# Optimization experiments

Measured on AMD Instinct MI355X. Metric: run time of the kernel, lower is better.

The kernel has to match this reference:

```python
import jax, jax.numpy as jnp
import numpy as np

B, C, H, W = 8, 128, 64, 64
KC = 32  # key_channels

def setup_inputs() -> dict:
    key = jax.random.key(0)
    ks = jax.random.split(key, 6)
    s = lambda fan_in: 1.0 / np.sqrt(fan_in)
    x  = jax.random.normal(ks[0], (B, C, H, W), dtype=jnp.float32)
    Wq = jax.random.uniform(ks[1], (KC, C), jnp.float32, -s(C), s(C))  # 1x1 conv kernels
    Wk = jax.random.uniform(ks[2], (KC, C), jnp.float32, -s(C), s(C))
    Wv = jax.random.uniform(ks[3], (C, C), jnp.float32, -s(C), s(C))
    Wo = jax.random.uniform(ks[4], (C, C), jnp.float32, -s(C), s(C))
    gamma = jnp.zeros((1,), jnp.float32) + 0.1  # nonzero so attention path matters
    return {"x": x, "Wq": Wq, "Wk": Wk, "Wv": Wv, "Wo": Wo, "gamma": gamma}

def reference(x, Wq, Wk, Wv, Wo, gamma):
    b, c, h, w = x.shape
    xf = x.reshape(b, c, h * w)                      # [B,C,N]
    Q = jnp.einsum('qc,bcn->bnq', Wq, xf)            # [B,N,KC]
    K = jnp.einsum('kc,bcn->bkn', Wk, xf)            # [B,KC,N]
    V = jnp.einsum('vc,bcn->bnv', Wv, xf)            # [B,N,C]
    scores = jnp.einsum('bnq,bqm->bnm', Q, K) / jnp.sqrt(jnp.asarray(Wq.shape[0], x.dtype))
    attn = jax.nn.softmax(scores, axis=-1)           # [B,N,N]
    out = jnp.einsum('bnm,bmv->bvn', attn, V)        # [B,C,N]
    out = jnp.einsum('oc,bcn->bon', Wo, out).reshape(b, c, h, w)
    return x + gamma * out
```

## Files before the change

kernel.cpp:

```cpp
#include <hip/hip_runtime.h>
#include <hip/hip_bf16.h>

#define BB 8
#define CC 128
#define NN 4096
#define KCQ 32

typedef unsigned short u16;
typedef unsigned int u32;
typedef unsigned char u8;
typedef __bf16 bf16x8 __attribute__((ext_vector_type(8)));
typedef float f32x4 __attribute__((ext_vector_type(4)));
typedef long i64;

typedef const __attribute__((address_space(1))) void gas_t;
typedef __attribute__((address_space(3))) void las_t;

__device__ __forceinline__ u16 f2bf(float f){
  u32 u = __builtin_bit_cast(u32, f);
  u32 r = u + 0x7FFFu + ((u >> 16) & 1u);
  return (u16)(r >> 16);
}
__device__ __forceinline__ u32 cvtpk(float lo, float hi){
  u32 r; asm("v_cvt_pk_bf16_f32 %0, %1, %2" : "=v"(r) : "v"(lo), "v"(hi)); return r;
}
__device__ __forceinline__ u32 pk_fp8x4(float a, float b, float c, float d){
  int v = 0;
  v = __builtin_amdgcn_cvt_pk_fp8_f32(a, b, v, false);
  v = __builtin_amdgcn_cvt_pk_fp8_f32(c, d, v, true);
  return (u32)v;
}
__device__ __forceinline__ void gload16(const void* g, void* l){
  __builtin_amdgcn_global_load_lds((gas_t*)g, (las_t*)l, 16, 0, 0);
}

__global__ __launch_bounds__(256) void k_prep_w(const float* Wq, const float* Wk,
                                                const float* Wv, const float* Wo,
                                                u16* wsq, u16* wsk, u16* wsv, u16* wso){
  int i = blockIdx.x * 256 + threadIdx.x;
  const float SC = 0.2550350f;
  if (i < 4096)       wsq[i]        = f2bf(Wq[i] * SC);
  else if (i < 8192)  wsk[i-4096]   = f2bf(Wk[i-4096]);
  else if (i < 24576) wsv[i-8192]   = f2bf(Wv[i-8192]);
  else if (i < 40960) wso[i-24576]  = f2bf(Wo[i-24576]);
}

__global__ __launch_bounds__(512) void k_projx(const float* x, const u16* wq, const u16* wk,
                                               const u16* wv, u16* Qm, u16* Km, u8* Vt8){
  __shared__ __align__(16) u16 xL[64*132];
  int b = blockIdx.x >> 6, nb = (blockIdx.x & 63) * 64;
  int t = threadIdx.x;
  int n = t & 63, cg = t >> 6;
  #pragma unroll
  for (int it = 0; it < 16; ++it){
    int c = it*8 + cg;
    xL[n*132 + c] = f2bf(x[((size_t)b*CC + c)*NN + nb + n]);
  }
  __syncthreads();
  int w = t >> 6, l = t & 63, a = l & 15, g = l >> 4;
  int ns = w >> 1, half = w & 1;
  int n0 = nb + ns*16;
  bf16x8 xa[4];
  #pragma unroll
  for (int kc = 0; kc < 4; ++kc)
    xa[kc] = *(const bf16x8*)(xL + (ns*16 + a)*132 + kc*32 + g*8);
  __syncthreads();

  u32* vbuf = (u32*)xL;
  auto Vjob = [&](int vt){
    f32x4 acc = {0.f,0.f,0.f,0.f};
    #pragma unroll
    for (int kc = 0; kc < 4; ++kc){
      bf16x8 wa = ((const bf16x8*)(wv + (size_t)(vt*16 + a) * CC))[kc*4 + g];
      acc = __builtin_amdgcn_mfma_f32_16x16x32_bf16(xa[kc], wa, acc, 0,0,0);
    }
    int row = vt*16 + a;
    vbuf[row*16 + ((ns ^ ((a>>1)&3)) << 2) + g] = pk_fp8x4(acc[0], acc[1], acc[2], acc[3]);
  };

  if (half == 0){
    #pragma unroll
    for (int qt = 0; qt < 2; ++qt){
      f32x4 accq = {0.f,0.f,0.f,0.f}, acck = {0.f,0.f,0.f,0.f};
      #pragma unroll
      for (int kc = 0; kc < 4; ++kc){
        bf16x8 wbq = ((const bf16x8*)(wq + (size_t)(qt*16 + a) * CC))[kc*4 + g];
        bf16x8 wbk = ((const bf16x8*)(wk + (size_t)(qt*16 + a) * CC))[kc*4 + g];
        accq = __builtin_amdgcn_mfma_f32_16x16x32_bf16(xa[kc], wbq, accq, 0,0,0);
        acck = __builtin_amdgcn_mfma_f32_16x16x32_bf16(xa[kc], wbk, acck, 0,0,0);
      }
      #pragma unroll
      for (int r = 0; r < 4; ++r){
        Qm[((size_t)b*NN + n0 + 4*g + r) * KCQ + qt*16 + a] = f2bf(accq[r]);
        Km[((size_t)b*NN + n0 + 4*g + r) * KCQ + qt*16 + a] = f2bf(acck[r]);
      }
    }
    Vjob(0); Vjob(1);
  } else {
    #pragma unroll
    for (int vt = 2; vt < 8; ++vt) Vjob(vt);
  }
  __syncthreads();
  {
    int row = t >> 2, ck = t & 3, key = (row >> 1) & 3;
    uint4 d = ((const uint4*)vbuf)[row*4 + (ck ^ key)];
    *(uint4*)(Vt8 + ((size_t)b*CC + row)*NN + nb + ck*16) = d;
  }
}

__global__ __launch_bounds__(512, 4) void k_attn(const u16* Qm, const u16* Km,
                                                 const u8* Vt8, const u16* wso,
                                                 const float* x, const float* gamma,
                                                 float* out){
  __shared__ __align__(16) char smem[65536];
  int bid = blockIdx.x;
  int b = bid & 7, qb = bid >> 3;
  int t0 = threadIdx.x;
  int l = t0 & 63, a = l & 15, g = l >> 4;
  int w = t0 >> 6, h = w >> 2, wq = w & 3;
  int q0 = qb * 64;
  int kb0 = h * 2048;

  const u8* Vb = Vt8 + (size_t)b * CC * NN;

  bf16x8 qf[4];
  #pragma unroll
  for (int qs = 0; qs < 4; ++qs)
    qf[qs] = ((const bf16x8*)(Qm + ((size_t)b*NN + q0 + qs*16 + a) * KCQ))[g];
  const u16* kPtr = Km + ((size_t)b*NN + kb0 + wq*16 + a) * KCQ + g*8;

  f32x4 o[8];
  #pragma unroll
  for (int i = 0; i < 8; ++i) o[i] = (f32x4){0.f,0.f,0.f,0.f};
  float ls[4] = {0.f, 0.f, 0.f, 0.f};

  int schk = (l&3) ^ ((l>>3)&3);
  const u8* vSrc = Vb + (size_t)(wq*32 + (l>>2))*NN + kb0 + (schk << 4);
  int vOff = h*8192 + wq*2048 + l*16;
  auto stageV = [&](int t1, int sl){
    const u8* vs = vSrc + t1*64;
    char* vd = smem + sl*16384 + vOff;
    gload16(vs, vd);
    gload16(vs + (size_t)16*NN, vd + 1024);
  };

  const int cswz = (a >> 1) & 3;
  auto PV = [&](int ps, int vsl){
    const char* Vs = smem + vsl*16384 + h*8192;
    const char* Pr = smem + 49152 + ps*8192 + h*4096;
    __builtin_amdgcn_s_setprio(1);
    #pragma unroll
    for (int kk = 0; kk < 2; ++kk){
      int kx = (((kk*2 + (g>>1)) ^ cswz) << 4) + (g&1)*8;
      i64 vf0 = *(const i64*)(Vs + (wq*32 + a)*64 + kx);
      i64 vf1 = *(const i64*)(Vs + (wq*32 + 16 + a)*64 + kx);
      i64 pf[4];
      #pragma unroll
      for (int qs = 0; qs < 4; ++qs)
        pf[qs] = *(const i64*)(Pr + (qs*16 + a)*64 + kx);
      #pragma unroll
      for (int qs = 0; qs < 4; ++qs){
        o[qs*2  ] = __builtin_amdgcn_mfma_f32_16x16x32_fp8_fp8(vf0, pf[qs], o[qs*2  ], 0,0,0);
        o[qs*2+1] = __builtin_amdgcn_mfma_f32_16x16x32_fp8_fp8(vf1, pf[qs], o[qs*2+1], 0,0,0);
      }
    }
    __builtin_amdgcn_s_setprio(0);
  };

  stageV(0, 0);
  bf16x8 kfC = *(const bf16x8*)(kPtr);

  int vS = 1, vR = 2;
  for (int t = 0; t < 32; ++t){
    bf16x8 kfN;
    if (t < 31){
      kfN = *(const bf16x8*)(kPtr + (size_t)(t+1)*2048);
      stageV(t+1, vS);
    }
    f32x4 sv[4];
    #pragma unroll
    for (int qs = 0; qs < 4; ++qs){
      f32x4 z = {0.f,0.f,0.f,0.f};
      sv[qs] = __builtin_amdgcn_mfma_f32_16x16x32_bf16(kfC, qf[qs], z, 0,0,0);
    }
    if (t > 0) PV((t&1)^1, vR);
    char* Pw = smem + 49152 + (t&1)*8192 + h*4096;
    #pragma unroll
    for (int qs = 0; qs < 4; ++qs){
      float p0 = __builtin_amdgcn_exp2f(sv[qs][0]);
      float p1 = __builtin_amdgcn_exp2f(sv[qs][1]);
      float p2 = __builtin_amdgcn_exp2f(sv[qs][2]);
      float p3 = __builtin_amdgcn_exp2f(sv[qs][3]);
      ls[qs] += (p0 + p1) + (p2 + p3);
      *(u32*)(Pw + (qs*16 + a)*64 + ((wq ^ cswz) << 4) + 4*g) = pk_fp8x4(p0, p1, p2, p3);
    }
    if (t < 31) { asm volatile("s_waitcnt vmcnt(3) lgkmcnt(0)" ::: "memory"); }
    else        { asm volatile("s_waitcnt vmcnt(0) lgkmcnt(0)" ::: "memory"); }
    __builtin_amdgcn_s_barrier();
    kfC = kfN;
    vR = (vR == 2) ? 0 : vR + 1;
    vS = (vS == 2) ? 0 : vS + 1;
  }
  PV(1, vR);

  #pragma unroll
  for (int qs = 0; qs < 4; ++qs){
    ls[qs] += __shfl_xor(ls[qs], 16);
    ls[qs] += __shfl_xor(ls[qs], 32);
  }
  float* Ml = (float*)(smem + 36864);
  if (l < 16){
    #pragma unroll
    for (int qs = 0; qs < 4; ++qs) Ml[w*64 + qs*16 + l] = ls[qs];
  }
  float* Cx = (float*)smem;
  __syncthreads();
  if (h == 1){
    #pragma unroll
    for (int i = 0; i < 8; ++i){
      int qs = i >> 1, st = i & 1;
      *(f32x4*)(Cx + (qs*16 + a)*132 + wq*32 + st*16 + 4*g) = o[i];
    }
  }
  __syncthreads();
  u16* Ol = (u16*)(smem + 49152);
  if (h == 0){
    #pragma unroll
    for (int qs = 0; qs < 4; ++qs){
      float lsum = 0.f;
      #pragma unroll
      for (int ww = 0; ww < 8; ++ww) lsum += Ml[ww*64 + qs*16 + a];
      float inv = 1.f / lsum;
      #pragma unroll
      for (int st = 0; st < 2; ++st){
        f32x4 oc = o[qs*2 + st];
        const float* cx = Cx + (qs*16 + a)*132 + wq*32 + st*16 + 4*g;
        uint2 pk;
        pk.x = cvtpk((oc[0] + cx[0]) * inv, (oc[1] + cx[1]) * inv);
        pk.y = cvtpk((oc[2] + cx[2]) * inv, (oc[3] + cx[3]) * inv);
        int chunk = (wq*4 + st*2 + (g>>1)) ^ (a & 7);
        *(uint2*)((char*)Ol + (qs*16 + a)*256 + chunk*16 + (g&1)*8) = pk;
      }
    }
  }
  __syncthreads();
  float gm = gamma[0];
  f32x4 acc2[4];
  #pragma unroll
  for (int qs = 0; qs < 4; ++qs) acc2[qs] = (f32x4){0.f,0.f,0.f,0.f};
  #pragma unroll
  for (int kc = 0; kc < 4; ++kc){
    bf16x8 wof = *(const bf16x8*)(wso + (size_t)(w*16 + a)*CC + kc*32 + g*8);
    #pragma unroll
    for (int qs = 0; qs < 4; ++qs){
      int chunk = (kc*4 + g) ^ (a & 7);
      bf16x8 of = *(const bf16x8*)((const char*)Ol + (qs*16 + a)*256 + chunk*16);
      acc2[qs] = __builtin_amdgcn_mfma_f32_16x16x32_bf16(wof, of, acc2[qs], 0,0,0);
    }
  }
  #pragma unroll
  for (int qs = 0; qs < 4; ++qs){
    #pragma unroll
    for (int r = 0; r < 4; ++r){
      size_t idx = ((size_t)b*CC + w*16 + 4*g + r)*NN + q0 + qs*16 + a;
      out[idx] = x[idx] + gm * acc2[qs][r];
    }
  }
}

extern "C" void kernel_launch(void* const* d_in, const int* in_sizes, int n_in,
                              void* d_out, int out_size, void* d_ws, size_t ws_size,
                              hipStream_t stream) {
  const float* x     = (const float*)d_in[0];
  const float* Wq    = (const float*)d_in[1];
  const float* Wk    = (const float*)d_in[2];
  const float* Wv    = (const float*)d_in[3];
  const float* Wo    = (const float*)d_in[4];
  const float* gamma = (const float*)d_in[5];
  float* out = (float*)d_out;

  u16* wsq = (u16*)d_ws;
  u16* wsk = wsq + 4096;
  u16* wsv = wsk + 4096;
  u16* wso = wsv + 16384;
  u16* Qm  = wso + 16384;
  u16* Km  = Qm + (size_t)BB*NN*KCQ;
  u8*  Vt8 = (u8*)(Km + (size_t)BB*NN*KCQ);

  hipLaunchKernelGGL(k_prep_w, dim3(160), dim3(256), 0, stream, Wq, Wk, Wv, Wo, wsq, wsk, wsv, wso);
  hipLaunchKernelGGL(k_projx,  dim3(512), dim3(512), 0, stream, x, wsq, wsk, wsv, Qm, Km, Vt8);
  hipLaunchKernelGGL(k_attn,   dim3(512), dim3(512), 0, stream, Qm, Km, Vt8, wso, x, gamma, out);
}
```

Measured before the change: 73.03 us.

## Restructure attention kernel to 32-query blocks with direct V register loads

Each attention block now handles 32 queries with 4 waves instead of 64 queries with 8 waves. The two-half key split, with its cross-half reduction of partial outputs through shared memory, is gone. V fp8 fragments are loaded straight from global memory into registers each iteration instead of being staged into LDS with a triple-buffered async copy, so LDS use drops to about 8.5 KB and the grid doubles to 1024 blocks. The aim is higher occupancy and less LDS traffic, at the cost of reading the full V of the batch twice as often from cache and exposing global load latency inside the loop.

```diff
diff --git a/kernel.cpp b/kernel.cpp
--- a/kernel.cpp
+++ b/kernel.cpp
@@ -13,9 +13,6 @@
 typedef float f32x4 __attribute__((ext_vector_type(4)));
 typedef long i64;
 
-typedef const __attribute__((address_space(1))) void gas_t;
-typedef __attribute__((address_space(3))) void las_t;
-
 __device__ __forceinline__ u16 f2bf(float f){
   u32 u = __builtin_bit_cast(u32, f);
   u32 r = u + 0x7FFFu + ((u >> 16) & 1u);
@@ -29,9 +26,6 @@
   v = __builtin_amdgcn_cvt_pk_fp8_f32(a, b, v, false);
   v = __builtin_amdgcn_cvt_pk_fp8_f32(c, d, v, true);
   return (u32)v;
-}
-__device__ __forceinline__ void gload16(const void* g, void* l){
-  __builtin_amdgcn_global_load_lds((gas_t*)g, (las_t*)l, 16, 0, 0);
 }
 
 __global__ __launch_bounds__(256) void k_prep_w(const float* Wq, const float* Wk,
@@ -108,164 +102,142 @@
   }
 }
 
-__global__ __launch_bounds__(512, 4) void k_attn(const u16* Qm, const u16* Km,
+__global__ __launch_bounds__(256, 4) void k_attn(const u16* Qm, const u16* Km,
                                                  const u8* Vt8, const u16* wso,
                                                  const float* x, const float* gamma,
                                                  float* out){
-  __shared__ __align__(16) char smem[65536];
+  __shared__ __align__(16) char smem[8704];
   int bid = blockIdx.x;
   int b = bid & 7, qb = bid >> 3;
   int t0 = threadIdx.x;
   int l = t0 & 63, a = l & 15, g = l >> 4;
-  int w = t0 >> 6, h = w >> 2, wq = w & 3;
-  int q0 = qb * 64;
-  int kb0 = h * 2048;
-
-  const u8* Vb = Vt8 + (size_t)b * CC * NN;
-
-  bf16x8 qf[4];
-  #pragma unroll
-  for (int qs = 0; qs < 4; ++qs)
+  int w = t0 >> 6;
+  int q0 = qb * 32;
+
+  bf16x8 qf[2];
+  #pragma unroll
+  for (int qs = 0; qs < 2; ++qs)
     qf[qs] = ((const bf16x8*)(Qm + ((size_t)b*NN + q0 + qs*16 + a) * KCQ))[g];
-  const u16* kPtr = Km + ((size_t)b*NN + kb0 + wq*16 + a) * KCQ + g*8;
-
-  f32x4 o[8];
-  #pragma unroll
-  for (int i = 0; i < 8; ++i) o[i] = (f32x4){0.f,0.f,0.f,0.f};
-  float ls[4] = {0.f, 0.f, 0.f, 0.f};
-
-  int schk = (l&3) ^ ((l>>3)&3);
-  const u8* vSrc = Vb + (size_t)(wq*32 + (l>>2))*NN + kb0 + (schk << 4);
-  int vOff = h*8192 + wq*2048 + l*16;
-  auto stageV = [&](int t1, int sl){
-    const u8* vs = vSrc + t1*64;
-    char* vd = smem + sl*16384 + vOff;
-    gload16(vs, vd);
-    gload16(vs + (size_t)16*NN, vd + 1024);
-  };
-
-  const int cswz = (a >> 1) & 3;
-  auto PV = [&](int ps, int vsl){
-    const char* Vs = smem + vsl*16384 + h*8192;
-    const char* Pr = smem + 49152 + ps*8192 + h*4096;
+
+  const u16* kPtr = Km + ((size_t)b*NN + w*32 + a) * KCQ + g*8;
+  const u8*  vP0  = Vt8 + ((size_t)b*CC + w*32 + a) * NN + g*8;
+  const u8*  vP1  = vP0 + (size_t)16 * NN;
+
+  f32x4 o[4];
+  #pragma unroll
+  for (int i = 0; i < 4; ++i) o[i] = (f32x4){0.f,0.f,0.f,0.f};
+  float ls[2] = {0.f, 0.f};
+
+  const int sx = (a & 7) << 4;
+  bf16x8 kfC[2];
+  kfC[0] = *(const bf16x8*)(kPtr);
+  kfC[1] = *(const bf16x8*)(kPtr + 512);
+
+  for (int t = 0; t < 32; ++t){
+    i64 vf[8];
+    #pragma unroll
+    for (int kk = 0; kk < 4; ++kk){
+      vf[kk]     = *(const i64*)(vP0 + t*128 + kk*32);
+      vf[4 + kk] = *(const i64*)(vP1 + t*128 + kk*32);
+    }
+    bf16x8 kfN[2];
+    kfN[0] = *(const bf16x8*)(kPtr + (size_t)(t+1)*4096);
+    kfN[1] = *(const bf16x8*)(kPtr + (size_t)(t+1)*4096 + 512);
+
+    f32x4 sv[4];
+    #pragma unroll
+    for (int su = 0; su < 2; ++su)
+      #pragma unroll
+      for (int qs = 0; qs < 2; ++qs){
+        f32x4 z = {0.f,0.f,0.f,0.f};
+        sv[su*2+qs] = __builtin_amdgcn_mfma_f32_16x16x32_bf16(kfC[su], qf[qs], z, 0,0,0);
+      }
+    char* Pw = smem + (t&1)*4096;
+    #pragma unroll
+    for (int su = 0; su < 2; ++su)
+      #pragma unroll
+      for (int qs = 0; qs < 2; ++qs){
+        f32x4 s = sv[su*2+qs];
+        float p0 = __builtin_amdgcn_exp2f(s[0]);
+        float p1 = __builtin_amdgcn_exp2f(s[1]);
+        float p2 = __builtin_amdgcn_exp2f(s[2]);
+        float p3 = __builtin_amdgcn_exp2f(s[3]);
+        ls[qs] += (p0 + p1) + (p2 + p3);
+        *(u32*)(Pw + (qs*16 + a)*128 + (((w*2 + su) << 4) ^ sx) + 4*g) =
+            pk_fp8x4(p0, p1, p2, p3);
+      }
+    asm volatile("s_waitcnt lgkmcnt(0)" ::: "memory");
+    __builtin_amdgcn_s_barrier();
+
+    const char* Pr = Pw;
     __builtin_amdgcn_s_setprio(1);
     #pragma unroll
-    for (int kk = 0; kk < 2; ++kk){
-      int kx = (((kk*2 + (g>>1)) ^ cswz) << 4) + (g&1)*8;
-      i64 vf0 = *(const i64*)(Vs + (wq*32 + a)*64 + kx);
-      i64 vf1 = *(const i64*)(Vs + (wq*32 + 16 + a)*64 + kx);
-      i64 pf[4];
-      #pragma unroll
-      for (int qs = 0; qs < 4; ++qs)
-        pf[qs] = *(const i64*)(Pr + (qs*16 + a)*64 + kx);
-      #pragma unroll
-      for (int qs = 0; qs < 4; ++qs){
-        o[qs*2  ] = __builtin_amdgcn_mfma_f32_16x16x32_fp8_fp8(vf0, pf[qs], o[qs*2  ], 0,0,0);
-        o[qs*2+1] = __builtin_amdgcn_mfma_f32_16x16x32_fp8_fp8(vf1, pf[qs], o[qs*2+1], 0,0,0);
-      }
+    for (int kk = 0; kk < 4; ++kk){
+      int kx = (((kk*2 + (g>>1)) << 4) ^ sx) + (g&1)*8;
+      i64 pf0 = *(const i64*)(Pr + a*128 + kx);
+      i64 pf1 = *(const i64*)(Pr + (16 + a)*128 + kx);
+      o[0] = __builtin_amdgcn_mfma_f32_16x16x32_fp8_fp8(vf[kk],   pf0, o[0], 0,0,0);
+      o[1] = __builtin_amdgcn_mfma_f32_16x16x32_fp8_fp8(vf[kk],   pf1, o[1], 0,0,0);
+      o[2] = __builtin_amdgcn_mfma_f32_16x16x32_fp8_fp8(vf[4+kk], pf0, o[2], 0,0,0);
+      o[3] = __builtin_amdgcn_mfma_f32_16x16x32_fp8_fp8(vf[4+kk], pf1, o[3], 0,0,0);
     }
     __builtin_amdgcn_s_setprio(0);
-  };
-
-  stageV(0, 0);
-  bf16x8 kfC = *(const bf16x8*)(kPtr);
-
-  int vS = 1, vR = 2;
-  for (int t = 0; t < 32; ++t){
-    bf16x8 kfN;
-    if (t < 31){
-      kfN = *(const bf16x8*)(kPtr + (size_t)(t+1)*2048);
-      stageV(t+1, vS);
-    }
-    f32x4 sv[4];
-    #pragma unroll
-    for (int qs = 0; qs < 4; ++qs){
-      f32x4 z = {0.f,0.f,0.f,0.f};
-      sv[qs] = __builtin_amdgcn_mfma_f32_16x16x32_bf16(kfC, qf[qs], z, 0,0,0);
-    }
-    if (t > 0) PV((t&1)^1, vR);
-    char* Pw = smem + 49152 + (t&1)*8192 + h*4096;
-    #pragma unroll
-    for (int qs = 0; qs < 4; ++qs){
-      float p0 = __builtin_amdgcn_exp2f(sv[qs][0]);
-      float p1 = __builtin_amdgcn_exp2f(sv[qs][1]);
-      float p2 = __builtin_amdgcn_exp2f(sv[qs][2]);
-      float p3 = __builtin_amdgcn_exp2f(sv[qs][3]);
-      ls[qs] += (p0 + p1) + (p2 + p3);
-      *(u32*)(Pw + (qs*16 + a)*64 + ((wq ^ cswz) << 4) + 4*g) = pk_fp8x4(p0, p1, p2, p3);
-    }
-    if (t < 31) { asm volatile("s_waitcnt vmcnt(3) lgkmcnt(0)" ::: "memory"); }
-    else        { asm volatile("s_waitcnt vmcnt(0) lgkmcnt(0)" ::: "memory"); }
-    __builtin_amdgcn_s_barrier();
-    kfC = kfN;
-    vR = (vR == 2) ? 0 : vR + 1;
-    vS = (vS == 2) ? 0 : vS + 1;
-  }
-  PV(1, vR);
-
-  #pragma unroll
-  for (int qs = 0; qs < 4; ++qs){
+    kfC[0] = kfN[0]; kfC[1] = kfN[1];
+  }
+
+  #pragma unroll
+  for (int qs = 0; qs < 2; ++qs){
     ls[qs] += __shfl_xor(ls[qs], 16);
     ls[qs] += __shfl_xor(ls[qs], 32);
   }
-  float* Ml = (float*)(smem + 36864);
+  float* Ml = (float*)(smem + 8192);
+  __syncthreads();
   if (l < 16){
-    #pragma unroll
-    for (int qs = 0; qs < 4; ++qs) Ml[w*64 + qs*16 + l] = ls[qs];
-  }
-  float* Cx = (float*)smem;
-  __syncthreads();
-  if (h == 1){
-    #pragma unroll
-    for (int i = 0; i < 8; ++i){
-      int qs = i >> 1, st = i & 1;
-      *(f32x4*)(Cx + (qs*16 + a)*132 + wq*32 + st*16 + 4*g) = o[i];
-    }
-  }
-  __syncthreads();
-  u16* Ol = (u16*)(smem + 49152);
-  if (h == 0){
-    #pragma unroll
-    for (int qs = 0; qs < 4; ++qs){
-      float lsum = 0.f;
-      #pragma unroll
-      for (int ww = 0; ww < 8; ++ww) lsum += Ml[ww*64 + qs*16 + a];
-      float inv = 1.f / lsum;
-      #pragma unroll
-      for (int st = 0; st < 2; ++st){
-        f32x4 oc = o[qs*2 + st];
-        const float* cx = Cx + (qs*16 + a)*132 + wq*32 + st*16 + 4*g;
-        uint2 pk;
-        pk.x = cvtpk((oc[0] + cx[0]) * inv, (oc[1] + cx[1]) * inv);
-        pk.y = cvtpk((oc[2] + cx[2]) * inv, (oc[3] + cx[3]) * inv);
-        int chunk = (wq*4 + st*2 + (g>>1)) ^ (a & 7);
-        *(uint2*)((char*)Ol + (qs*16 + a)*256 + chunk*16 + (g&1)*8) = pk;
-      }
+    Ml[w*32 + l]      = ls[0];
+    Ml[w*32 + 16 + l] = ls[1];
+  }
+  __syncthreads();
+  u16* Ol = (u16*)smem;
+  #pragma unroll
+  for (int qs = 0; qs < 2; ++qs){
+    float lsum = Ml[qs*16 + a] + Ml[32 + qs*16 + a] + Ml[64 + qs*16 + a] + Ml[96 + qs*16 + a];
+    float inv = 1.f / lsum;
+    #pragma unroll
+    for (int st = 0; st < 2; ++st){
+      f32x4 oc = o[st*2 + qs];
+      uint2 pk;
+      pk.x = cvtpk(oc[0]*inv, oc[1]*inv);
+      pk.y = cvtpk(oc[2]*inv, oc[3]*inv);
+      int chunk = (w*4 + st*2 + (g>>1)) ^ (a & 7);
+      *(uint2*)((char*)Ol + (qs*16 + a)*256 + chunk*16 + (g&1)*8) = pk;
     }
   }
   __syncthreads();
   float gm = gamma[0];
   f32x4 acc2[4];
   #pragma unroll
-  for (int qs = 0; qs < 4; ++qs) acc2[qs] = (f32x4){0.f,0.f,0.f,0.f};
+  for (int i = 0; i < 4; ++i) acc2[i] = (f32x4){0.f,0.f,0.f,0.f};
   #pragma unroll
   for (int kc = 0; kc < 4; ++kc){
-    bf16x8 wof = *(const bf16x8*)(wso + (size_t)(w*16 + a)*CC + kc*32 + g*8);
-    #pragma unroll
-    for (int qs = 0; qs < 4; ++qs){
+    bf16x8 wof0 = *(const bf16x8*)(wso + (size_t)(w*32 + a)*CC + kc*32 + g*8);
+    bf16x8 wof1 = *(const bf16x8*)(wso + (size_t)(w*32 + 16 + a)*CC + kc*32 + g*8);
+    #pragma unroll
+    for (int qs = 0; qs < 2; ++qs){
       int chunk = (kc*4 + g) ^ (a & 7);
       bf16x8 of = *(const bf16x8*)((const char*)Ol + (qs*16 + a)*256 + chunk*16);
-      acc2[qs] = __builtin_amdgcn_mfma_f32_16x16x32_bf16(wof, of, acc2[qs], 0,0,0);
-    }
-  }
-  #pragma unroll
-  for (int qs = 0; qs < 4; ++qs){
-    #pragma unroll
-    for (int r = 0; r < 4; ++r){
-      size_t idx = ((size_t)b*CC + w*16 + 4*g + r)*NN + q0 + qs*16 + a;
-      out[idx] = x[idx] + gm * acc2[qs][r];
-    }
-  }
+      acc2[qs]     = __builtin_amdgcn_mfma_f32_16x16x32_bf16(wof0, of, acc2[qs],     0,0,0);
+      acc2[2 + qs] = __builtin_amdgcn_mfma_f32_16x16x32_bf16(wof1, of, acc2[2 + qs], 0,0,0);
+    }
+  }
+  #pragma unroll
+  for (int st = 0; st < 2; ++st)
+    #pragma unroll
+    for (int qs = 0; qs < 2; ++qs)
+      #pragma unroll
+      for (int r = 0; r < 4; ++r){
+        size_t idx = ((size_t)b*CC + w*32 + st*16 + 4*g + r)*NN + q0 + qs*16 + a;
+        out[idx] = x[idx] + gm * acc2[st*2 + qs][r];
+      }
 }
 
 extern "C" void kernel_launch(void* const* d_in, const int* in_sizes, int n_in,
@@ -287,7 +259,7 @@
   u16* Km  = Qm + (size_t)BB*NN*KCQ;
   u8*  Vt8 = (u8*)(Km + (size_t)BB*NN*KCQ);
 
-  hipLaunchKernelGGL(k_prep_w, dim3(160), dim3(256), 0, stream, Wq, Wk, Wv, Wo, wsq, wsk, wsv, wso);
-  hipLaunchKernelGGL(k_projx,  dim3(512), dim3(512), 0, stream, x, wsq, wsk, wsv, Qm, Km, Vt8);
-  hipLaunchKernelGGL(k_attn,   dim3(512), dim3(512), 0, stream, Qm, Km, Vt8, wso, x, gamma, out);
-}
+  hipLaunchKernelGGL(k_prep_w, dim3(160),  dim3(256), 0, stream, Wq, Wk, Wv, Wo, wsq, wsk, wsv, wso);
+  hipLaunchKernelGGL(k_projx,  dim3(512),  dim3(512), 0, stream, x, wsq, wsk, wsv, Qm, Km, Vt8);
+  hipLaunchKernelGGL(k_attn,   dim3(1024), dim3(256), 0, stream, Qm, Km, Vt8, wso, x, gamma, out);
+}
```

Result: slower. 161.5 us (+121.1%).

## Halve attention query tile to 32 and simplify V staging to double buffer

Applied to the files above, without the earlier changes.

The attention kernel now handles 32 queries per block instead of 64, doubling the grid to 1024 blocks and cutting LDS to 40KB with launch bounds raised to 8 waves per EU for more blocks per CU. The V pipeline moves from a triple-buffered prefetch, where PV lagged one step behind, to a double buffer: the next V tile is issued after the barrier and PV is consumed in the same iteration. This trades more K/V reloads per query (less reuse) for higher occupancy and a simpler schedule. It also risks exposing load latency, since the PV of each step now waits on the barrier.

```diff
diff --git a/kernel.cpp b/kernel.cpp
--- a/kernel.cpp
+++ b/kernel.cpp
@@ -108,85 +108,56 @@
   }
 }
 
-__global__ __launch_bounds__(512, 4) void k_attn(const u16* Qm, const u16* Km,
+__global__ __launch_bounds__(512, 8) void k_attn(const u16* Qm, const u16* Km,
                                                  const u8* Vt8, const u16* wso,
                                                  const float* x, const float* gamma,
                                                  float* out){
-  __shared__ __align__(16) char smem[65536];
+  __shared__ __align__(16) char smem[40960];
   int bid = blockIdx.x;
   int b = bid & 7, qb = bid >> 3;
   int t0 = threadIdx.x;
   int l = t0 & 63, a = l & 15, g = l >> 4;
   int w = t0 >> 6, h = w >> 2, wq = w & 3;
-  int q0 = qb * 64;
-  int kb0 = h * 2048;
-
-  const u8* Vb = Vt8 + (size_t)b * CC * NN;
-
-  bf16x8 qf[4];
-  #pragma unroll
-  for (int qs = 0; qs < 4; ++qs)
+  int q0 = qb * 32;
+
+  bf16x8 qf[2];
+  #pragma unroll
+  for (int qs = 0; qs < 2; ++qs)
     qf[qs] = ((const bf16x8*)(Qm + ((size_t)b*NN + q0 + qs*16 + a) * KCQ))[g];
-  const u16* kPtr = Km + ((size_t)b*NN + kb0 + wq*16 + a) * KCQ + g*8;
-
-  f32x4 o[8];
-  #pragma unroll
-  for (int i = 0; i < 8; ++i) o[i] = (f32x4){0.f,0.f,0.f,0.f};
-  float ls[4] = {0.f, 0.f, 0.f, 0.f};
+
+  const u16* kRun = Km + ((size_t)b*NN + h*2048 + wq*16 + a) * KCQ + g*8;
+
+  f32x4 o[4];
+  #pragma unroll
+  for (int i = 0; i < 4; ++i) o[i] = (f32x4){0.f,0.f,0.f,0.f};
+  float ls[2] = {0.f, 0.f};
 
   int schk = (l&3) ^ ((l>>3)&3);
-  const u8* vSrc = Vb + (size_t)(wq*32 + (l>>2))*NN + kb0 + (schk << 4);
-  int vOff = h*8192 + wq*2048 + l*16;
-  auto stageV = [&](int t1, int sl){
-    const u8* vs = vSrc + t1*64;
-    char* vd = smem + sl*16384 + vOff;
-    gload16(vs, vd);
-    gload16(vs + (size_t)16*NN, vd + 1024);
-  };
+  const u8* vRun = Vt8 + (size_t)b*CC*NN + (size_t)(wq*32 + (l>>2))*NN + h*2048 + schk*16;
+  const int vOff = h*8192 + wq*2048 + l*16;
+
+  {
+    char* vd = smem + vOff;
+    gload16(vRun, vd);
+    gload16(vRun + (size_t)16*NN, vd + 1024);
+    vRun += 64;
+  }
+  bf16x8 kfC = *(const bf16x8*)kRun; kRun += 2048;
 
   const int cswz = (a >> 1) & 3;
-  auto PV = [&](int ps, int vsl){
-    const char* Vs = smem + vsl*16384 + h*8192;
-    const char* Pr = smem + 49152 + ps*8192 + h*4096;
-    __builtin_amdgcn_s_setprio(1);
-    #pragma unroll
-    for (int kk = 0; kk < 2; ++kk){
-      int kx = (((kk*2 + (g>>1)) ^ cswz) << 4) + (g&1)*8;
-      i64 vf0 = *(const i64*)(Vs + (wq*32 + a)*64 + kx);
-      i64 vf1 = *(const i64*)(Vs + (wq*32 + 16 + a)*64 + kx);
-      i64 pf[4];
-      #pragma unroll
-      for (int qs = 0; qs < 4; ++qs)
-        pf[qs] = *(const i64*)(Pr + (qs*16 + a)*64 + kx);
-      #pragma unroll
-      for (int qs = 0; qs < 4; ++qs){
-        o[qs*2  ] = __builtin_amdgcn_mfma_f32_16x16x32_fp8_fp8(vf0, pf[qs], o[qs*2  ], 0,0,0);
-        o[qs*2+1] = __builtin_amdgcn_mfma_f32_16x16x32_fp8_fp8(vf1, pf[qs], o[qs*2+1], 0,0,0);
-      }
-    }
-    __builtin_amdgcn_s_setprio(0);
-  };
-
-  stageV(0, 0);
-  bf16x8 kfC = *(const bf16x8*)(kPtr);
-
-  int vS = 1, vR = 2;
+
   for (int t = 0; t < 32; ++t){
-    bf16x8 kfN;
-    if (t < 31){
-      kfN = *(const bf16x8*)(kPtr + (size_t)(t+1)*2048);
-      stageV(t+1, vS);
-    }
-    f32x4 sv[4];
-    #pragma unroll
-    for (int qs = 0; qs < 4; ++qs){
+    bf16x8 kfN = *(const bf16x8*)kRun; kRun += 2048;
+
+    f32x4 sv[2];
+    #pragma unroll
+    for (int qs = 0; qs < 2; ++qs){
       f32x4 z = {0.f,0.f,0.f,0.f};
       sv[qs] = __builtin_amdgcn_mfma_f32_16x16x32_bf16(kfC, qf[qs], z, 0,0,0);
     }
-    if (t > 0) PV((t&1)^1, vR);
-    char* Pw = smem + 49152 + (t&1)*8192 + h*4096;
-    #pragma unroll
-    for (int qs = 0; qs < 4; ++qs){
+    char* Pw = smem + 32768 + (t&1)*4096 + h*2048;
+    #pragma unroll
+    for (int qs = 0; qs < 2; ++qs){
       float p0 = __builtin_amdgcn_exp2f(sv[qs][0]);
       float p1 = __builtin_amdgcn_exp2f(sv[qs][1]);
       float p2 = __builtin_amdgcn_exp2f(sv[qs][2]);
@@ -194,46 +165,66 @@
       ls[qs] += (p0 + p1) + (p2 + p3);
       *(u32*)(Pw + (qs*16 + a)*64 + ((wq ^ cswz) << 4) + 4*g) = pk_fp8x4(p0, p1, p2, p3);
     }
-    if (t < 31) { asm volatile("s_waitcnt vmcnt(3) lgkmcnt(0)" ::: "memory"); }
+    if (t < 31) { asm volatile("s_waitcnt vmcnt(1) lgkmcnt(0)" ::: "memory"); }
     else        { asm volatile("s_waitcnt vmcnt(0) lgkmcnt(0)" ::: "memory"); }
     __builtin_amdgcn_s_barrier();
+
+    if (t < 31){
+      char* vd = smem + (((t+1)&1) << 14) + vOff;
+      gload16(vRun, vd);
+      gload16(vRun + (size_t)16*NN, vd + 1024);
+      vRun += 64;
+    }
+    const char* Vs = smem + ((t&1) << 14) + h*8192;
+    const char* Pr = smem + 32768 + (t&1)*4096 + h*2048;
+    __builtin_amdgcn_s_setprio(1);
+    #pragma unroll
+    for (int kk = 0; kk < 2; ++kk){
+      int kx = (((kk*2 + (g>>1)) ^ cswz) << 4) + (g&1)*8;
+      i64 pf0 = *(const i64*)(Pr + a*64 + kx);
+      i64 pf1 = *(const i64*)(Pr + (16 + a)*64 + kx);
+      i64 vf0 = *(const i64*)(Vs + (wq*32 + a)*64 + kx);
+      i64 vf1 = *(const i64*)(Vs + (wq*32 + 16 + a)*64 + kx);
+      o[0] = __builtin_amdgcn_mfma_f32_16x16x32_fp8_fp8(vf0, pf0, o[0], 0,0,0);
+      o[1] = __builtin_amdgcn_mfma_f32_16x16x32_fp8_fp8(vf0, pf1, o[1], 0,0,0);
+      o[2] = __builtin_amdgcn_mfma_f32_16x16x32_fp8_fp8(vf1, pf0, o[2], 0,0,0);
+      o[3] = __builtin_amdgcn_mfma_f32_16x16x32_fp8_fp8(vf1, pf1, o[3], 0,0,0);
+    }
+    __builtin_amdgcn_s_setprio(0);
     kfC = kfN;
-    vR = (vR == 2) ? 0 : vR + 1;
-    vS = (vS == 2) ? 0 : vS + 1;
-  }
-  PV(1, vR);
-
-  #pragma unroll
-  for (int qs = 0; qs < 4; ++qs){
+  }
+
+  #pragma unroll
+  for (int qs = 0; qs < 2; ++qs){
     ls[qs] += __shfl_xor(ls[qs], 16);
     ls[qs] += __shfl_xor(ls[qs], 32);
   }
-  float* Ml = (float*)(smem + 36864);
+  __syncthreads();
+  float* Ml = (float*)(smem + 32768);
   if (l < 16){
-    #pragma unroll
-    for (int qs = 0; qs < 4; ++qs) Ml[w*64 + qs*16 + l] = ls[qs];
+    Ml[w*32 + l]      = ls[0];
+    Ml[w*32 + 16 + l] = ls[1];
   }
   float* Cx = (float*)smem;
-  __syncthreads();
   if (h == 1){
     #pragma unroll
-    for (int i = 0; i < 8; ++i){
-      int qs = i >> 1, st = i & 1;
-      *(f32x4*)(Cx + (qs*16 + a)*132 + wq*32 + st*16 + 4*g) = o[i];
-    }
-  }
-  __syncthreads();
-  u16* Ol = (u16*)(smem + 49152);
+    for (int st = 0; st < 2; ++st)
+      #pragma unroll
+      for (int qs = 0; qs < 2; ++qs)
+        *(f32x4*)(Cx + (qs*16 + a)*132 + wq*32 + st*16 + 4*g) = o[st*2 + qs];
+  }
+  __syncthreads();
+  u16* Ol = (u16*)(smem + 17408);
   if (h == 0){
     #pragma unroll
-    for (int qs = 0; qs < 4; ++qs){
+    for (int qs = 0; qs < 2; ++qs){
       float lsum = 0.f;
       #pragma unroll
-      for (int ww = 0; ww < 8; ++ww) lsum += Ml[ww*64 + qs*16 + a];
+      for (int ww = 0; ww < 8; ++ww) lsum += Ml[ww*32 + qs*16 + a];
       float inv = 1.f / lsum;
       #pragma unroll
       for (int st = 0; st < 2; ++st){
-        f32x4 oc = o[qs*2 + st];
+        f32x4 oc = o[st*2 + qs];
         const float* cx = Cx + (qs*16 + a)*132 + wq*32 + st*16 + 4*g;
         uint2 pk;
         pk.x = cvtpk((oc[0] + cx[0]) * inv, (oc[1] + cx[1]) * inv);
@@ -245,27 +236,26 @@
   }
   __syncthreads();
   float gm = gamma[0];
-  f32x4 acc2[4];
-  #pragma unroll
-  for (int qs = 0; qs < 4; ++qs) acc2[qs] = (f32x4){0.f,0.f,0.f,0.f};
+  f32x4 acc2[2];
+  acc2[0] = (f32x4){0.f,0.f,0.f,0.f};
+  acc2[1] = (f32x4){0.f,0.f,0.f,0.f};
   #pragma unroll
   for (int kc = 0; kc < 4; ++kc){
     bf16x8 wof = *(const bf16x8*)(wso + (size_t)(w*16 + a)*CC + kc*32 + g*8);
     #pragma unroll
-    for (int qs = 0; qs < 4; ++qs){
+    for (int qs = 0; qs < 2; ++qs){
       int chunk = (kc*4 + g) ^ (a & 7);
       bf16x8 of = *(const bf16x8*)((const char*)Ol + (qs*16 + a)*256 + chunk*16);
       acc2[qs] = __builtin_amdgcn_mfma_f32_16x16x32_bf16(wof, of, acc2[qs], 0,0,0);
     }
   }
   #pragma unroll
-  for (int qs = 0; qs < 4; ++qs){
+  for (int qs = 0; qs < 2; ++qs)
     #pragma unroll
     for (int r = 0; r < 4; ++r){
       size_t idx = ((size_t)b*CC + w*16 + 4*g + r)*NN + q0 + qs*16 + a;
       out[idx] = x[idx] + gm * acc2[qs][r];
     }
-  }
 }
 
 extern "C" void kernel_launch(void* const* d_in, const int* in_sizes, int n_in,
@@ -287,7 +277,7 @@
   u16* Km  = Qm + (size_t)BB*NN*KCQ;
   u8*  Vt8 = (u8*)(Km + (size_t)BB*NN*KCQ);
 
-  hipLaunchKernelGGL(k_prep_w, dim3(160), dim3(256), 0, stream, Wq, Wk, Wv, Wo, wsq, wsk, wsv, wso);
-  hipLaunchKernelGGL(k_projx,  dim3(512), dim3(512), 0, stream, x, wsq, wsk, wsv, Qm, Km, Vt8);
-  hipLaunchKernelGGL(k_attn,   dim3(512), dim3(512), 0, stream, Qm, Km, Vt8, wso, x, gamma, out);
-}
+  hipLaunchKernelGGL(k_prep_w, dim3(160),  dim3(256), 0, stream, Wq, Wk, Wv, Wo, wsq, wsk, wsv, wso);
+  hipLaunchKernelGGL(k_projx,  dim3(512),  dim3(512), 0, stream, x, wsq, wsk, wsv, Qm, Km, Vt8);
+  hipLaunchKernelGGL(k_attn,   dim3(1024), dim3(512), 0, stream, Qm, Km, Vt8, wso, x, gamma, out);
+}
```

New measurement: 82.76 us. +13.3%, slower.
